# Optimization experiments

Measured on AMD Instinct MI355X. Metric: run time of the kernel, lower is better.

The kernel has to match this reference:

```python
import jax, jax.numpy as jnp
import numpy as np

OUTPUT_SIZE = 256  # D: softmax / reduction dim (init arg output_size)


def setup_inputs() -> dict:
    key = jax.random.key(0)
    k1, k2 = jax.random.split(key)
    S = jax.random.normal(k1, (8192, OUTPUT_SIZE), dtype=jnp.float32)
    V = jax.random.normal(k2, (8192, OUTPUT_SIZE), dtype=jnp.float32)
    return {"S": S, "V": V}


def reference(S, V):
    # Original torch module: S, V viewed to (-1, D); for each pair (i, j)
    # it runs an online-softmax (flash-attention style) recurrence over D,
    # computing O[i, j] = sum_k softmax(S[i])_k * V[j, k].
    # Vectorized: O = softmax(S, -1) @ V.T  -> shape [N, M]
    D = S.shape[-1]
    S2 = S.reshape(-1, D)  # [N, D]
    V2 = V.reshape(-1, D)  # [M, D]
    P = jax.nn.softmax(S2, axis=-1)  # stable online-softmax equivalent
    return jnp.einsum('nd,md->nm', P, V2)
```

## Files before the change

### kernel.cpp

```cpp
#include <hip/hip_runtime.h>

typedef __attribute__((ext_vector_type(8))) short bf16x8;
typedef __attribute__((ext_vector_type(4))) float f32x4;

#define D_DIM 256
#define NROW  8192

__device__ __forceinline__ unsigned short f2bf(float x) {
  unsigned int u = __float_as_uint(x);
  u += 0x7fffu + ((u >> 16) & 1u);
  return (unsigned short)(u >> 16);
}

__device__ __forceinline__ void gload_lds16(const void* g, void* l) {
  __builtin_amdgcn_global_load_lds((__attribute__((address_space(1))) void*)g,
                                   (__attribute__((address_space(3))) void*)l,
                                   16, 0, 0);
}

__global__ __launch_bounds__(256) void softmax_rows(const float* __restrict__ S,
                                                    unsigned short* __restrict__ P) {
  const int row  = blockIdx.x * 4 + (threadIdx.x >> 6);
  const int lane = threadIdx.x & 63;
  float4 v = ((const float4*)(S + row * D_DIM))[lane];
  float m = fmaxf(fmaxf(v.x, v.y), fmaxf(v.z, v.w));
#pragma unroll
  for (int off = 32; off > 0; off >>= 1) m = fmaxf(m, __shfl_xor(m, off));
  float e0 = __expf(v.x - m), e1 = __expf(v.y - m);
  float e2 = __expf(v.z - m), e3 = __expf(v.w - m);
  float s = e0 + e1 + e2 + e3;
#pragma unroll
  for (int off = 32; off > 0; off >>= 1) s += __shfl_xor(s, off);
  const float inv = 1.0f / s;
  ushort4 o;
  o.x = f2bf(e0 * inv); o.y = f2bf(e1 * inv);
  o.z = f2bf(e2 * inv); o.w = f2bf(e3 * inv);
  ((ushort4*)(P + row * D_DIM))[lane] = o;
}

__global__ __launch_bounds__(256) void cast_v(const float* __restrict__ V,
                                              unsigned short* __restrict__ Vb) {
  const int i = blockIdx.x * 256 + threadIdx.x;
  float4 v = ((const float4*)V)[i];
  ushort4 o;
  o.x = f2bf(v.x); o.y = f2bf(v.y); o.z = f2bf(v.z); o.w = f2bf(v.w);
  ((ushort4*)Vb)[i] = o;
}

__global__ __launch_bounds__(256) void gemm_bt(const unsigned short* __restrict__ P,
                                               const unsigned short* __restrict__ Vb,
                                               float* __restrict__ O) {
  __shared__ float smem[8704];
  unsigned short* As = (unsigned short*)smem;
  unsigned short* Bs = (unsigned short*)smem + 4096;

  const int t    = threadIdx.x;
  const int lane = t & 63;
  const int wave = t >> 6;
  const int wm   = (wave & 1) * 64;
  const int wn   = (wave >> 1) * 64;
  const int bm   = blockIdx.x;
  const int bn   = blockIdx.y;

  f32x4 acc[4][4] = {};

  const int srow = t >> 2;
  const int scol = (t & 3) * 8;
  const unsigned short* ga = P  + (bm * 128 + srow) * D_DIM + scol;
  const unsigned short* gb = Vb + (bn * 128 + srow) * D_DIM + scol;
  unsigned short* la = As + srow * 32 + scol;
  unsigned short* lb = Bs + srow * 32 + scol;

  const int arow = wm + (lane & 15);
  const int brow = wn + (lane & 15);
  const int koff = (lane >> 4) * 8;

  for (int k0 = 0; k0 < D_DIM; k0 += 32) {
    gload_lds16(ga + k0,              la);
    gload_lds16(ga + 64 * D_DIM + k0, la + 64 * 32);
    gload_lds16(gb + k0,              lb);
    gload_lds16(gb + 64 * D_DIM + k0, lb + 64 * 32);
    __syncthreads();

    bf16x8 af[4], bfr[4];
#pragma unroll
    for (int mi = 0; mi < 4; ++mi)
      af[mi] = *(const bf16x8*)&As[(arow + mi * 16) * 32 + koff];
#pragma unroll
    for (int ni = 0; ni < 4; ++ni)
      bfr[ni] = *(const bf16x8*)&Bs[(brow + ni * 16) * 32 + koff];

#pragma unroll
    for (int mi = 0; mi < 4; ++mi)
#pragma unroll
      for (int ni = 0; ni < 4; ++ni)
        acc[mi][ni] = __builtin_amdgcn_mfma_f32_16x16x32_bf16(af[mi], bfr[ni],
                                                              acc[mi][ni], 0, 0, 0);
    __syncthreads();
  }

  float* ep = smem + wave * 2176;
  const int qrow = (lane >> 4) * 4;
  const int qcol = lane & 15;
  const size_t orow0 = (size_t)(bm * 128 + wm);
  const int    ocol0 = bn * 128 + wn + (lane & 15) * 4;

#pragma unroll
  for (int p = 0; p < 2; ++p) {
#pragma unroll
    for (int mi2 = 0; mi2 < 2; ++mi2) {
      const int mi = p * 2 + mi2;
      const int r0 = mi2 * 16 + qrow;
#pragma unroll
      for (int ni = 0; ni < 4; ++ni)
#pragma unroll
        for (int r = 0; r < 4; ++r)
          ep[(r0 + r) * 68 + ni * 16 + qcol] = acc[mi][ni][r];
    }
#pragma unroll
    for (int q = 0; q < 8; ++q) {
      const int rl = q * 4 + (lane >> 4);
      float4 vv = *(const float4*)&ep[rl * 68 + (lane & 15) * 4];
      *(float4*)&O[(orow0 + p * 32 + rl) * NROW + ocol0] = vv;
    }
    if (p == 0) __syncthreads();
  }
}

extern "C" void kernel_launch(void* const* d_in, const int* in_sizes, int n_in,
                              void* d_out, int out_size, void* d_ws, size_t ws_size,
                              hipStream_t stream) {
  const float* S = (const float*)d_in[0];
  const float* V = (const float*)d_in[1];
  float* O = (float*)d_out;

  unsigned short* P  = (unsigned short*)d_ws;
  unsigned short* Vb = P + (size_t)NROW * D_DIM;

  softmax_rows<<<NROW / 4, 256, 0, stream>>>(S, P);
  cast_v<<<(NROW * D_DIM / 4) / 256, 256, 0, stream>>>(V, Vb);
  gemm_bt<<<dim3(NROW / 128, NROW / 128), 256, 0, stream>>>(P, Vb, O);
}
```

Baseline: 293.9 us.

## Double-buffer GEMM K tiles with XOR-swizzled LDS and XCD-aware block mapping

The GEMM mainloop now uses K-tiles of 64 with two LDS buffers, so the global-to-LDS loads for the next tile are issued while MFMAs run on the current one. Each loop previously paid two block barriers. LDS rows are XOR-swizzled to avoid bank conflicts on the fragment reads. A 1D grid is remapped so blocks on the same XCD share rows of P, improving L2 reuse. LDS use grows to 64KB per block, which may reduce occupancy.

```diff
diff --git a/kernel.cpp b/kernel.cpp
--- a/kernel.cpp
+++ b/kernel.cpp
@@ -47,59 +47,104 @@
   ((ushort4*)Vb)[i] = o;
 }
 
+
+__device__ __forceinline__ void stage_tile(const unsigned short* ga,
+                                           const unsigned short* gb,
+                                           unsigned short* la, int ko) {
+  gload_lds16(ga + ko,              la);
+  gload_lds16(ga + 32 * D_DIM + ko, la + 2048);
+  gload_lds16(ga + 64 * D_DIM + ko, la + 4096);
+  gload_lds16(ga + 96 * D_DIM + ko, la + 6144);
+  gload_lds16(gb + ko,              la + 8192);
+  gload_lds16(gb + 32 * D_DIM + ko, la + 8192 + 2048);
+  gload_lds16(gb + 64 * D_DIM + ko, la + 8192 + 4096);
+  gload_lds16(gb + 96 * D_DIM + ko, la + 8192 + 6144);
+}
+
+__device__ __forceinline__ void compute_tile(const unsigned short* __restrict__ A_,
+                                             const unsigned short* __restrict__ B_,
+                                             int arow, int brow, int k16,
+                                             f32x4 acc[4][4]) {
+#pragma unroll
+  for (int j = 0; j < 2; ++j) {
+    bf16x8 af[4], bfr[4];
+#pragma unroll
+    for (int mi = 0; mi < 4; ++mi) {
+      const int r = arow + mi * 16;
+      af[mi] = *(const bf16x8*)&A_[r * 64 + ((j * 32 + k16) ^ ((r & 7) * 8))];
+    }
+#pragma unroll
+    for (int ni = 0; ni < 4; ++ni) {
+      const int r = brow + ni * 16;
+      bfr[ni] = *(const bf16x8*)&B_[r * 64 + ((j * 32 + k16) ^ ((r & 7) * 8))];
+    }
+#pragma unroll
+    for (int mi = 0; mi < 4; ++mi)
+#pragma unroll
+      for (int ni = 0; ni < 4; ++ni)
+        acc[mi][ni] = __builtin_amdgcn_mfma_f32_16x16x32_bf16(af[mi], bfr[ni],
+                                                              acc[mi][ni], 0, 0, 0);
+  }
+}
+
 __global__ __launch_bounds__(256) void gemm_bt(const unsigned short* __restrict__ P,
                                                const unsigned short* __restrict__ Vb,
                                                float* __restrict__ O) {
-  __shared__ float smem[8704];
-  unsigned short* As = (unsigned short*)smem;
-  unsigned short* Bs = (unsigned short*)smem + 4096;
+  __shared__ unsigned short smem[32768];
 
   const int t    = threadIdx.x;
   const int lane = t & 63;
   const int wave = t >> 6;
   const int wm   = (wave & 1) * 64;
   const int wn   = (wave >> 1) * 64;
-  const int bm   = blockIdx.x;
-  const int bn   = blockIdx.y;
+
+  const int id  = blockIdx.x;
+  const int xcd = id & 7;
+  const int q   = id >> 3;
+  const int bm  = xcd * 8 + (q & 7);
+  const int bn  = q >> 3;
 
   f32x4 acc[4][4] = {};
 
-  const int srow = t >> 2;
-  const int scol = (t & 3) * 8;
-  const unsigned short* ga = P  + (bm * 128 + srow) * D_DIM + scol;
-  const unsigned short* gb = Vb + (bn * 128 + srow) * D_DIM + scol;
-  unsigned short* la = As + srow * 32 + scol;
-  unsigned short* lb = Bs + srow * 32 + scol;
+  const int srow = t >> 3;
+  const int xg   = ((t & 7) * 8) ^ ((srow & 7) * 8);
+  const unsigned short* ga = P  + (size_t)(bm * 128 + srow) * D_DIM + xg;
+  const unsigned short* gb = Vb + (size_t)(bn * 128 + srow) * D_DIM + xg;
+  unsigned short* l0 = smem + t * 8;
 
   const int arow = wm + (lane & 15);
   const int brow = wn + (lane & 15);
-  const int koff = (lane >> 4) * 8;
+  const int k16  = (lane >> 4) * 8;
 
-  for (int k0 = 0; k0 < D_DIM; k0 += 32) {
-    gload_lds16(ga + k0,              la);
-    gload_lds16(ga + 64 * D_DIM + k0, la + 64 * 32);
-    gload_lds16(gb + k0,              lb);
-    gload_lds16(gb + 64 * D_DIM + k0, lb + 64 * 32);
-    __syncthreads();
+  stage_tile(ga, gb, l0, 0);
+  asm volatile("s_waitcnt vmcnt(0)" ::: "memory");
+  __builtin_amdgcn_s_barrier();
+  __builtin_amdgcn_sched_barrier(0);
 
-    bf16x8 af[4], bfr[4];
-#pragma unroll
-    for (int mi = 0; mi < 4; ++mi)
-      af[mi] = *(const bf16x8*)&As[(arow + mi * 16) * 32 + koff];
-#pragma unroll
-    for (int ni = 0; ni < 4; ++ni)
-      bfr[ni] = *(const bf16x8*)&Bs[(brow + ni * 16) * 32 + koff];
+  stage_tile(ga, gb, l0 + 16384, 64);
+  compute_tile(smem, smem + 8192, arow, brow, k16, acc);
+  asm volatile("s_waitcnt vmcnt(0)" ::: "memory");
+  __builtin_amdgcn_s_barrier();
+  __builtin_amdgcn_sched_barrier(0);
 
-#pragma unroll
-    for (int mi = 0; mi < 4; ++mi)
-#pragma unroll
-      for (int ni = 0; ni < 4; ++ni)
-        acc[mi][ni] = __builtin_amdgcn_mfma_f32_16x16x32_bf16(af[mi], bfr[ni],
-                                                              acc[mi][ni], 0, 0, 0);
-    __syncthreads();
-  }
+  stage_tile(ga, gb, l0, 128);
+  compute_tile(smem + 16384, smem + 24576, arow, brow, k16, acc);
+  asm volatile("s_waitcnt vmcnt(0)" ::: "memory");
+  __builtin_amdgcn_s_barrier();
+  __builtin_amdgcn_sched_barrier(0);
 
-  float* ep = smem + wave * 2176;
+  stage_tile(ga, gb, l0 + 16384, 192);
+  compute_tile(smem, smem + 8192, arow, brow, k16, acc);
+  asm volatile("s_waitcnt vmcnt(0)" ::: "memory");
+  __builtin_amdgcn_s_barrier();
+  __builtin_amdgcn_sched_barrier(0);
+
+  compute_tile(smem + 16384, smem + 24576, arow, brow, k16, acc);
+
+  __syncthreads();
+
+  float* smf = (float*)smem;
+  float* ep  = smf + wave * 2176;
   const int qrow = (lane >> 4) * 4;
   const int qcol = lane & 15;
   const size_t orow0 = (size_t)(bm * 128 + wm);
@@ -118,8 +163,8 @@
           ep[(r0 + r) * 68 + ni * 16 + qcol] = acc[mi][ni][r];
     }
 #pragma unroll
-    for (int q = 0; q < 8; ++q) {
-      const int rl = q * 4 + (lane >> 4);
+    for (int qq = 0; qq < 8; ++qq) {
+      const int rl = qq * 4 + (lane >> 4);
       float4 vv = *(const float4*)&ep[rl * 68 + (lane & 15) * 4];
       *(float4*)&O[(orow0 + p * 32 + rl) * NROW + ocol0] = vv;
     }
@@ -139,5 +184,5 @@
 
   softmax_rows<<<NROW / 4, 256, 0, stream>>>(S, P);
   cast_v<<<(NROW * D_DIM / 4) / 256, 256, 0, stream>>>(V, Vb);
-  gemm_bt<<<dim3(NROW / 128, NROW / 128), 256, 0, stream>>>(P, Vb, O);
+  gemm_bt<<<NROW / 128 * (NROW / 128), 256, 0, stream>>>(P, Vb, O);
 }
```

New measurement: 289.2 us. Within noise of the previous version (-1.6%).
